# Kernel optimization log

Hardware: AMD Instinct MI355X
Metric: run time of the kernel (lower is better)

## Reference

```python
import jax, jax.numpy as jnp
import numpy as np

N_HEAD = 16


def setup_inputs() -> dict:
    key = jax.random.key(0)
    k1, k2, k3 = jax.random.split(key, 3)
    B, S, D = 2, 2048, 1024
    return {
        "hidden_states": jax.random.normal(k1, (B, S, D), dtype=jnp.float32),
        "c_attn_w": jax.random.normal(k2, (D, 3 * D), dtype=jnp.float32) * 0.02,
        "c_attn_b": jnp.zeros((3 * D,), dtype=jnp.float32),
        "c_proj_w": jax.random.normal(k3, (D, D), dtype=jnp.float32) * 0.02,
        "c_proj_b": jnp.zeros((D,), dtype=jnp.float32),
    }


def reference(hidden_states, c_attn_w, c_attn_b, c_proj_w, c_proj_b):
    B, S, D = hidden_states.shape
    H = N_HEAD
    hd = D // H
    # Fused QKV projection (Conv1D == linear with transposed weight layout)
    qkv = hidden_states @ c_attn_w + c_attn_b  # [B,S,3D]
    q, k, v = jnp.split(qkv, 3, axis=-1)
    # split heads -> [B,H,S,hd]
    q = q.reshape(B, S, H, hd).transpose(0, 2, 1, 3)
    k = k.reshape(B, S, H, hd).transpose(0, 2, 1, 3)
    v = v.reshape(B, S, H, hd).transpose(0, 2, 1, 3)
    # scaled dot-product with causal mask
    scores = jnp.einsum("bhqd,bhkd->bhqk", q, k) / jnp.asarray(hd ** 0.5, q.dtype)
    causal = jnp.tril(jnp.ones((S, S), dtype=bool))  # [S,S]
    mask_value = jnp.finfo(scores.dtype).min
    scores = jnp.where(causal[None, None, :, :], scores, mask_value)
    attn_weights = jax.nn.softmax(scores, axis=-1)  # [B,H,S,S]
    ctx = jnp.einsum("bhqk,bhkd->bhqd", attn_weights, v)  # [B,H,S,hd]
    ctx = ctx.transpose(0, 2, 1, 3).reshape(B, S, D)  # merge heads
    out = ctx @ c_proj_w + c_proj_b  # [B,S,D]
    return out
```

## Files before the change

### kernel.cpp

```cpp
#include <hip/hip_runtime.h>
#include <hip/hip_bf16.h>

typedef __attribute__((ext_vector_type(8))) short short8;
typedef __attribute__((ext_vector_type(4))) float f32x4;
typedef __attribute__((ext_vector_type(16))) float f32x16;
typedef __attribute__((ext_vector_type(4))) unsigned short u16x4;
typedef __attribute__((ext_vector_type(4))) unsigned int u32x4;

#define MFMA16(a, b, c) __builtin_amdgcn_mfma_f32_16x16x32_bf16((a), (b), (c), 0, 0, 0)
#define MFMA32(a, b, c) __builtin_amdgcn_mfma_f32_32x32x16_bf16((a), (b), (c), 0, 0, 0)

__device__ __forceinline__ unsigned short f2bf(float f) {
    union { float f; unsigned u; } v; v.f = f;
    return (unsigned short)((v.u + 0x7fffu + ((v.u >> 16) & 1u)) >> 16);
}

__device__ __forceinline__ unsigned cvtpk(float lo, float hi_) {
    unsigned r;
    asm volatile("v_cvt_pk_bf16_f32 %0, %1, %2" : "=v"(r) : "v"(lo), "v"(hi_));
    return r;
}

__global__ void cast_x_kernel(const float* __restrict__ x, ushort* __restrict__ y) {
    int i = blockIdx.x * blockDim.x + threadIdx.x;
    float4 v = ((const float4*)x)[i];
    u16x4 o = { f2bf(v.x), f2bf(v.y), f2bf(v.z), f2bf(v.w) };
    *(u16x4*)(y + (size_t)i * 4) = o;
}

__global__ void transpose_cast_kernel(const float* __restrict__ W, ushort* __restrict__ WT,
                                      int K, int N) {
    __shared__ ushort t[64][66];
    int n0 = blockIdx.x * 64, k0 = blockIdx.y * 64;
    int tn = threadIdx.x & 63, tg = threadIdx.x >> 6;
#pragma unroll
    for (int i = 0; i < 16; ++i) {
        int k = tg * 16 + i;
        t[tn][k] = f2bf(W[(size_t)(k0 + k) * N + n0 + tn]);
    }
    __syncthreads();
#pragma unroll
    for (int i = 0; i < 16; ++i) {
        int nn = tg * 16 + i;
        WT[(size_t)(n0 + nn) * K + k0 + tn] = t[nn][tn];
    }
}

#define QSCALE 0.18033688011112042f

template <int MODE>
__global__ __launch_bounds__(256, 3)
void gemm_bt_kernel(const ushort* __restrict__ A, const ushort* __restrict__ BT,
                    const float* __restrict__ bias,
                    ushort* __restrict__ Qb, ushort* __restrict__ Kb,
                    ushort* __restrict__ VT, float* __restrict__ Out,
                    int M, int N, int K) {
    __shared__ ushort Asm[2][128 * 32];
    __shared__ ushort Bsm[2][128 * 32];
    const int tid = threadIdx.x;
    const int lane = tid & 63;
    const int wv = tid >> 6;
    const int l15 = lane & 15, lg = lane >> 4;
    const int rm = (wv >> 1) * 64, cn = (wv & 1) * 64;
    const int row0 = blockIdx.y * 128, col0 = blockIdx.x * 128;

    const char* Agb = (const char*)(A + (size_t)row0 * K);
    const char* Bgb = (const char*)(BT + (size_t)col0 * K);
    const size_t rowbytes = (size_t)K * 2;

    f32x4 acc[4][4];
#pragma unroll
    for (int mi = 0; mi < 4; ++mi)
#pragma unroll
        for (int ni = 0; ni < 4; ++ni) acc[mi][ni] = f32x4{0.f, 0.f, 0.f, 0.f};

    const int sr0 = tid >> 2, sc0 = (tid & 3) ^ (sr0 & 3);
    const int sr1 = (tid + 256) >> 2, sc1 = (tid & 3) ^ (sr1 & 3);

#define GSTAGE(buf, k0_)                                                                \
    do {                                                                                \
        size_t kbyte = (size_t)(k0_)*2;                                                 \
        __builtin_amdgcn_global_load_lds(                                               \
            (const __attribute__((address_space(1))) void*)(Agb + (size_t)sr0 *         \
                rowbytes + kbyte + sc0 * 16),                                           \
            (__attribute__((address_space(3))) void*)((char*)&Asm[buf][0] + tid * 16),  \
            16, 0, 0);                                                                  \
        __builtin_amdgcn_global_load_lds(                                               \
            (const __attribute__((address_space(1))) void*)(Agb + (size_t)sr1 *         \
                rowbytes + kbyte + sc1 * 16),                                           \
            (__attribute__((address_space(3))) void*)((char*)&Asm[buf][0] + 4096 +      \
                tid * 16),                                                              \
            16, 0, 0);                                                                  \
        __builtin_amdgcn_global_load_lds(                                               \
            (const __attribute__((address_space(1))) void*)(Bgb + (size_t)sr0 *         \
                rowbytes + kbyte + sc0 * 16),                                           \
            (__attribute__((address_space(3))) void*)((char*)&Bsm[buf][0] + tid * 16),  \
            16, 0, 0);                                                                  \
        __builtin_amdgcn_global_load_lds(                                               \
            (const __attribute__((address_space(1))) void*)(Bgb + (size_t)sr1 *         \
                rowbytes + kbyte + sc1 * 16),                                           \
            (__attribute__((address_space(3))) void*)((char*)&Bsm[buf][0] + 4096 +      \
                tid * 16),                                                              \
            16, 0, 0);                                                                  \
    } while (0)

    GSTAGE(0, 0);
    __syncthreads();

    const int sw8 = (lg ^ (l15 & 3)) << 3;

    int cur = 0;
    for (int k0 = 0; k0 < K; k0 += 32) {
        if (k0 + 32 < K) GSTAGE(cur ^ 1, k0 + 32);
        short8 af[4], bf[4];
#pragma unroll
        for (int mi = 0; mi < 4; ++mi)
            af[mi] = *(const short8*)&Asm[cur][(rm + mi * 16 + l15) * 32 + sw8];
#pragma unroll
        for (int ni = 0; ni < 4; ++ni)
            bf[ni] = *(const short8*)&Bsm[cur][(cn + ni * 16 + l15) * 32 + sw8];
        __builtin_amdgcn_s_setprio(1);
#pragma unroll
        for (int mi = 0; mi < 4; ++mi)
#pragma unroll
            for (int ni = 0; ni < 4; ++ni)
                acc[mi][ni] = MFMA16(af[mi], bf[ni], acc[mi][ni]);
        __builtin_amdgcn_s_setprio(0);
        __syncthreads();
        cur ^= 1;
    }
#undef GSTAGE

    if (MODE == 0) {
        const int sect = col0 >> 10;
#pragma unroll
        for (int ni = 0; ni < 4; ++ni) {
            int col = col0 + cn + ni * 16 + l15;
            float bv = bias[col];
            int dcol = col & 1023, h = dcol >> 6, dd = dcol & 63;
#pragma unroll
            for (int mi = 0; mi < 4; ++mi) {
                int mrow0 = row0 + rm + mi * 16 + lg * 4;
                if (sect == 2) {
                    int b = mrow0 >> 11, s = mrow0 & 2047;
                    u16x4 o;
#pragma unroll
                    for (int j = 0; j < 4; ++j) o[j] = f2bf(acc[mi][ni][j] + bv);
                    *(u16x4*)&VT[((size_t)((b << 4) + h) * 64 + dd) * 2048 + s] = o;
                } else {
                    ushort* dst = sect ? Kb : Qb;
                    float sc = sect ? 1.f : QSCALE;
#pragma unroll
                    for (int j = 0; j < 4; ++j) {
                        int tok = mrow0 + j;
                        int b = tok >> 11, s = tok & 2047;
                        dst[((size_t)((b << 4) + h) * 2048 + s) * 64 + dd] =
                            f2bf((acc[mi][ni][j] + bv) * sc);
                    }
                }
            }
        }
    } else {
#pragma unroll
        for (int ni = 0; ni < 4; ++ni) {
            int col = col0 + cn + ni * 16 + l15;
            float bv = bias[col];
#pragma unroll
            for (int mi = 0; mi < 4; ++mi) {
                int mrow0 = row0 + rm + mi * 16 + lg * 4;
#pragma unroll
                for (int j = 0; j < 4; ++j)
                    Out[(size_t)(mrow0 + j) * N + col] = acc[mi][ni][j] + bv;
            }
        }
    }
}

__global__ __launch_bounds__(256)
void attn_kernel(const ushort* __restrict__ Qb, const ushort* __restrict__ Kb,
                 const ushort* __restrict__ VT, ushort* __restrict__ CTX) {
    __shared__ __align__(16) ushort Ksm[2][64 * 64];
    __shared__ __align__(16) ushort Vsm[2][64 * 64];

    const int tid = threadIdx.x;
    const int lane = tid & 63;
    const int w = tid >> 6;
    const int l31 = lane & 31;
    const int hi = lane >> 5;
    const int r7 = l31 & 7;

    const int id = blockIdx.x;
    const int xcd = id & 7, jj = id >> 3;
    const int bh = (xcd << 2) + (jj >> 4);
    const int qt = ((jj >> 5) & 1) ? (jj & 15) : 15 - (jj & 15);
    const int qw0 = qt * 128 + w * 32;
    const int qrow = qw0 + l31;

    const ushort* Qh = Qb + (size_t)bh * 2048 * 64;
    const ushort* Kh = Kb + (size_t)bh * 2048 * 64;
    const ushort* Vh = VT + (size_t)bh * 64 * 2048;

    short8 qf[4];
#pragma unroll
    for (int dc = 0; dc < 4; ++dc)
        qf[dc] = *(const short8*)&Qh[(size_t)qrow * 64 + dc * 16 + hi * 8];

    const int srow = tid >> 3;
    const int scol = tid & 7;
    const int swz8 = (scol ^ (srow & 7)) * 8;

    u32x4 kr0, kr1, vr0, vr1;

#define LDREGS(kb_)                                                                     \
    do {                                                                                \
        const ushort* kp = Kh + (size_t)((kb_) + srow) * 64 + scol * 8;                 \
        kr0 = *(const u32x4*)kp;                                                        \
        kr1 = *(const u32x4*)(kp + 32 * 64);                                            \
        const ushort* vp = Vh + (size_t)srow * 2048 + (kb_) + scol * 8;                 \
        vr0 = *(const u32x4*)vp;                                                        \
        vr1 = *(const u32x4*)(vp + (size_t)32 * 2048);                                  \
    } while (0)

#define DSWRITE(buf)                                                                    \
    do {                                                                                \
        ushort* kd = &Ksm[buf][srow * 64 + swz8];                                       \
        *(u32x4*)kd = kr0;                                                              \
        *(u32x4*)(kd + 32 * 64) = kr1;                                                  \
        ushort* vd = &Vsm[buf][srow * 64 + swz8];                                       \
        *(u32x4*)vd = vr0;                                                              \
        *(u32x4*)(vd + 32 * 64) = vr1;                                                  \
    } while (0)

    const int nc = 2 * qt + 2;
    const int cdiag = 2 * qt + (w >> 1);

    LDREGS(0);
    DSWRITE(0);
    __syncthreads();

    float mrun = -1e30f, lsum = 0.f;
    f32x16 acc0, acc1;
#pragma unroll
    for (int r = 0; r < 16; ++r) { acc0[r] = 0.f; acc1[r] = 0.f; }

    int cur = 0;
    for (int c = 0; c < nc; ++c) {
        const int kb = c * 64;
        const bool havenext = (c + 1 < nc);
        if (havenext) LDREGS(kb + 64);

        if (!(w < 2 && c == nc - 1)) {
            const ushort* Kc = &Ksm[cur][0];
            const ushort* Vc = &Vsm[cur][0];

            short8 kf0[4], kf1[4];
#pragma unroll
            for (int dc = 0; dc < 4; ++dc) {
                kf0[dc] = *(const short8*)(Kc + l31 * 64 + (((dc * 2 + hi) ^ r7) << 3));
                kf1[dc] = *(const short8*)(Kc + (32 + l31) * 64 + (((dc * 2 + hi) ^ r7) << 3));
            }

            f32x16 st0, st1;
#pragma unroll
            for (int r = 0; r < 16; ++r) { st0[r] = 0.f; st1[r] = 0.f; }
            __builtin_amdgcn_s_setprio(1);
#pragma unroll
            for (int dc = 0; dc < 4; ++dc) {
                st0 = MFMA32(kf0[dc], qf[dc], st0);
                st1 = MFMA32(kf1[dc], qf[dc], st1);
            }
            __builtin_amdgcn_s_setprio(0);

            if (c == cdiag) {
                const int base0 = kb + (hi << 2);
                const int base1 = kb + 32 + (hi << 2);
#pragma unroll
                for (int r = 0; r < 16; ++r) {
                    int k0 = base0 + ((r & 3) + 8 * (r >> 2));
                    int k1 = base1 + ((r & 3) + 8 * (r >> 2));
                    st0[r] = (k0 <= qrow) ? st0[r] : -1e30f;
                    st1[r] = (k1 <= qrow) ? st1[r] : -1e30f;
                }
            }

            short8 vg0[4], vg1[4];
#pragma unroll
            for (int g = 0; g < 4; ++g) {
                vg0[g] = *(const short8*)(Vc + l31 * 64 + (((2 * g + hi) ^ r7) << 3));
                vg1[g] = *(const short8*)(Vc + (32 + l31) * 64 + (((2 * g + hi) ^ r7) << 3));
            }

            float tm[8];
#pragma unroll
            for (int i = 0; i < 8; ++i)
                tm[i] = fmaxf(fmaxf(st0[i], st0[i + 8]), fmaxf(st1[i], st1[i + 8]));
            float tmax = fmaxf(fmaxf(fmaxf(tm[0], tm[1]), fmaxf(tm[2], tm[3])),
                               fmaxf(fmaxf(tm[4], tm[5]), fmaxf(tm[6], tm[7])));
            tmax = fmaxf(tmax, __shfl_xor(tmax, 32));

            if (!__all(tmax <= mrun + 8.0f)) {
                float mnew = fmaxf(mrun, tmax);
                float sc = exp2f(mrun - mnew);
#pragma unroll
                for (int r = 0; r < 16; ++r) { acc0[r] *= sc; acc1[r] *= sc; }
                lsum *= sc;
                mrun = mnew;
            }

#pragma unroll
            for (int r = 0; r < 16; ++r) st0[r] = exp2f(st0[r] - mrun);
#pragma unroll
            for (int r = 0; r < 16; ++r) st1[r] = exp2f(st1[r] - mrun);
            float ts[8];
#pragma unroll
            for (int i = 0; i < 8; ++i) ts[i] = st0[i] + st0[i + 8];
#pragma unroll
            for (int i = 0; i < 8; ++i) ts[i] += st1[i] + st1[i + 8];
            float tsum = ((ts[0] + ts[1]) + (ts[2] + ts[3])) +
                         ((ts[4] + ts[5]) + (ts[6] + ts[7]));
            lsum += tsum;

            if (havenext) DSWRITE(cur ^ 1);

#define MAKE_PFRAG(st, kcL, out)                                                        \
    do {                                                                                \
        unsigned c00 = cvtpk(st[8 * kcL + 0], st[8 * kcL + 1]);                         \
        unsigned c01 = cvtpk(st[8 * kcL + 2], st[8 * kcL + 3]);                         \
        unsigned c10 = cvtpk(st[8 * kcL + 4], st[8 * kcL + 5]);                         \
        unsigned c11 = cvtpk(st[8 * kcL + 6], st[8 * kcL + 7]);                         \
        unsigned e0 = hi ? c00 : c10, e1 = hi ? c01 : c11;                              \
        unsigned pa0 = e0, pb0 = e0, pa1 = e1, pb1 = e1;                                \
        asm volatile("v_permlane32_swap_b32 %0, %1" : "+v"(pa0), "+v"(pb0));            \
        asm volatile("v_permlane32_swap_b32 %0, %1" : "+v"(pa1), "+v"(pb1));            \
        unsigned rec0 = hi ? pa0 : pb0;                                                 \
        unsigned rec1 = hi ? pa1 : pb1;                                                 \
        u32x4 fw;                                                                       \
        fw.x = hi ? rec0 : c00;                                                         \
        fw.y = hi ? rec1 : c01;                                                         \
        fw.z = hi ? c10 : rec0;                                                         \
        fw.w = hi ? c11 : rec1;                                                         \
        out = __builtin_bit_cast(short8, fw);                                           \
    } while (0)

            short8 pf;
            __builtin_amdgcn_s_setprio(1);
            MAKE_PFRAG(st0, 0, pf);
            acc0 = MFMA32(vg0[0], pf, acc0);
            acc1 = MFMA32(vg1[0], pf, acc1);
            MAKE_PFRAG(st0, 1, pf);
            acc0 = MFMA32(vg0[1], pf, acc0);
            acc1 = MFMA32(vg1[1], pf, acc1);
            MAKE_PFRAG(st1, 0, pf);
            acc0 = MFMA32(vg0[2], pf, acc0);
            acc1 = MFMA32(vg1[2], pf, acc1);
            MAKE_PFRAG(st1, 1, pf);
            acc0 = MFMA32(vg0[3], pf, acc0);
            acc1 = MFMA32(vg1[3], pf, acc1);
            __builtin_amdgcn_s_setprio(0);
#undef MAKE_PFRAG
        } else {
            if (havenext) DSWRITE(cur ^ 1);
        }

        __syncthreads();
        cur ^= 1;
    }
#undef LDREGS
#undef DSWRITE

    lsum += __shfl_xor(lsum, 32);
    const float inv = 1.f / lsum;
    const int b = bh >> 4, h = bh & 15;
    const size_t tokrow = ((size_t)b * 2048 + qw0 + l31) * 1024 + (size_t)h * 64;

#define WRITE_DT(accv, dt)                                                              \
    do {                                                                                \
        _Pragma("unroll")                                                               \
        for (int q2 = 0; q2 < 4; ++q2) {                                                \
            int d0 = dt * 32 + 8 * q2 + (hi << 2);                                      \
            u16x4 o;                                                                    \
            _Pragma("unroll")                                                           \
            for (int j = 0; j < 4; ++j) o[j] = f2bf(accv[4 * q2 + j] * inv);            \
            *(u16x4*)&CTX[tokrow + d0] = o;                                             \
        }                                                                               \
    } while (0)

    WRITE_DT(acc0, 0);
    WRITE_DT(acc1, 1);
#undef WRITE_DT
}

extern "C" void kernel_launch(void* const* d_in, const int* in_sizes, int n_in,
                              void* d_out, int out_size, void* d_ws, size_t ws_size,
                              hipStream_t stream) {
    const float* X     = (const float*)d_in[0];
    const float* Wqkv  = (const float*)d_in[1];
    const float* bqkv  = (const float*)d_in[2];
    const float* Wproj = (const float*)d_in[3];
    const float* bproj = (const float*)d_in[4];
    float* Out = (float*)d_out;

    ushort* Xb     = (ushort*)d_ws;
    ushort* WqkvT  = Xb + (size_t)4096 * 1024;
    ushort* WprojT = WqkvT + (size_t)3072 * 1024;
    ushort* Qb     = WprojT + (size_t)1024 * 1024;
    ushort* Kb     = Qb + (size_t)4096 * 1024;
    ushort* VT     = Kb + (size_t)4096 * 1024;
    ushort* CTX    = VT + (size_t)4096 * 1024;

    cast_x_kernel<<<4096, 256, 0, stream>>>(X, Xb);
    transpose_cast_kernel<<<dim3(48, 16), 256, 0, stream>>>(Wqkv, WqkvT, 1024, 3072);
    transpose_cast_kernel<<<dim3(16, 16), 256, 0, stream>>>(Wproj, WprojT, 1024, 1024);
    gemm_bt_kernel<0><<<dim3(24, 32), 256, 0, stream>>>(Xb, WqkvT, bqkv, Qb, Kb, VT, nullptr,
                                                        4096, 3072, 1024);
    attn_kernel<<<512, 256, 0, stream>>>(Qb, Kb, VT, CTX);
    gemm_bt_kernel<1><<<dim3(8, 32), 256, 0, stream>>>(CTX, WprojT, bproj, nullptr, nullptr,
                                                       nullptr, Out, 4096, 1024, 1024);
}
```

Before: 130.5 us.

## Split attention KV range across two blocks and merge partial results

Each causal query tile's key range is split into two halves processed by separate blocks (1024 blocks instead of 512). Each block writes fp32 partial outputs and running max/sum to workspace, and a new merge kernel combines them into bf16 context. This is meant to balance the causal workload across more workgroups and raise occupancy, with launch bounds now requesting 4 blocks per CU. The cost is extra fp32 traffic to workspace and one more kernel launch. The P-fragment construction is also simplified to feed cvtpk outputs straight into permlane32 swaps without the select logic.

```diff
diff --git a/kernel.cpp b/kernel.cpp
--- a/kernel.cpp
+++ b/kernel.cpp
@@ -176,9 +176,11 @@
     }
 }
 
-__global__ __launch_bounds__(256)
+template <int SPLIT>
+__global__ __launch_bounds__(256, 4)
 void attn_kernel(const ushort* __restrict__ Qb, const ushort* __restrict__ Kb,
-                 const ushort* __restrict__ VT, ushort* __restrict__ CTX) {
+                 const ushort* __restrict__ VT, ushort* __restrict__ CTX,
+                 float* __restrict__ OP, float* __restrict__ ML) {
     __shared__ __align__(16) ushort Ksm[2][64 * 64];
     __shared__ __align__(16) ushort Vsm[2][64 * 64];
 
@@ -190,9 +192,23 @@
     const int r7 = l31 & 7;
 
     const int id = blockIdx.x;
-    const int xcd = id & 7, jj = id >> 3;
-    const int bh = (xcd << 2) + (jj >> 4);
-    const int qt = ((jj >> 5) & 1) ? (jj & 15) : 15 - (jj & 15);
+    int bh, qt, half, cBeg, cEnd;
+    if (SPLIT) {
+        const int xcd = id & 7, jj = id >> 3;
+        bh = (xcd << 2) + (jj & 3);
+        const int r = jj >> 2;
+        half = r >> 4;
+        const int s = r & 15;
+        qt = (s < 8) ? s : 23 - s;
+        cBeg = half * (qt + 1);
+        cEnd = cBeg + (qt + 1);
+    } else {
+        const int xcd = id & 7, jj = id >> 3;
+        bh = (xcd << 2) + (jj >> 4);
+        qt = ((jj >> 5) & 1) ? (jj & 15) : 15 - (jj & 15);
+        half = 0; cBeg = 0; cEnd = 2 * qt + 2;
+    }
+    const int nc = 2 * qt + 2;
     const int qw0 = qt * 128 + w * 32;
     const int qrow = qw0 + l31;
 
@@ -231,10 +247,9 @@
         *(u32x4*)(vd + 32 * 64) = vr1;                                                  \
     } while (0)
 
-    const int nc = 2 * qt + 2;
     const int cdiag = 2 * qt + (w >> 1);
 
-    LDREGS(0);
+    LDREGS(cBeg * 64);
     DSWRITE(0);
     __syncthreads();
 
@@ -244,9 +259,9 @@
     for (int r = 0; r < 16; ++r) { acc0[r] = 0.f; acc1[r] = 0.f; }
 
     int cur = 0;
-    for (int c = 0; c < nc; ++c) {
+    for (int c = cBeg; c < cEnd; ++c) {
         const int kb = c * 64;
-        const bool havenext = (c + 1 < nc);
+        const bool havenext = (c + 1 < cEnd);
         if (havenext) LDREGS(kb + 64);
 
         if (!(w < 2 && c == nc - 1)) {
@@ -324,21 +339,14 @@
 
 #define MAKE_PFRAG(st, kcL, out)                                                        \
     do {                                                                                \
-        unsigned c00 = cvtpk(st[8 * kcL + 0], st[8 * kcL + 1]);                         \
-        unsigned c01 = cvtpk(st[8 * kcL + 2], st[8 * kcL + 3]);                         \
-        unsigned c10 = cvtpk(st[8 * kcL + 4], st[8 * kcL + 5]);                         \
-        unsigned c11 = cvtpk(st[8 * kcL + 6], st[8 * kcL + 7]);                         \
-        unsigned e0 = hi ? c00 : c10, e1 = hi ? c01 : c11;                              \
-        unsigned pa0 = e0, pb0 = e0, pa1 = e1, pb1 = e1;                                \
-        asm volatile("v_permlane32_swap_b32 %0, %1" : "+v"(pa0), "+v"(pb0));            \
-        asm volatile("v_permlane32_swap_b32 %0, %1" : "+v"(pa1), "+v"(pb1));            \
-        unsigned rec0 = hi ? pa0 : pb0;                                                 \
-        unsigned rec1 = hi ? pa1 : pb1;                                                 \
+        unsigned a0 = cvtpk(st[8 * kcL + 0], st[8 * kcL + 1]);                          \
+        unsigned a1 = cvtpk(st[8 * kcL + 2], st[8 * kcL + 3]);                          \
+        unsigned b0 = cvtpk(st[8 * kcL + 4], st[8 * kcL + 5]);                          \
+        unsigned b1 = cvtpk(st[8 * kcL + 6], st[8 * kcL + 7]);                          \
+        asm volatile("v_permlane32_swap_b32 %0, %1" : "+v"(a0), "+v"(b0));              \
+        asm volatile("v_permlane32_swap_b32 %0, %1" : "+v"(a1), "+v"(b1));              \
         u32x4 fw;                                                                       \
-        fw.x = hi ? rec0 : c00;                                                         \
-        fw.y = hi ? rec1 : c01;                                                         \
-        fw.z = hi ? c10 : rec0;                                                         \
-        fw.w = hi ? c11 : rec1;                                                         \
+        fw.x = a0; fw.y = a1; fw.z = b0; fw.w = b1;                                     \
         out = __builtin_bit_cast(short8, fw);                                           \
     } while (0)
 
@@ -369,10 +377,31 @@
 #undef DSWRITE
 
     lsum += __shfl_xor(lsum, 32);
-    const float inv = 1.f / lsum;
-    const int b = bh >> 4, h = bh & 15;
-    const size_t tokrow = ((size_t)b * 2048 + qw0 + l31) * 1024 + (size_t)h * 64;
-
+
+    if (SPLIT) {
+        const int pidx = ((bh << 4) + qt) * 2 + half;
+        float* op = OP + (size_t)pidx * 8192 + (size_t)(w * 32 + l31) * 64;
+#define WRITE_PART(accv, dt)                                                            \
+    do {                                                                                \
+        _Pragma("unroll")                                                               \
+        for (int q2 = 0; q2 < 4; ++q2) {                                                \
+            int d0 = dt * 32 + 8 * q2 + (hi << 2);                                      \
+            f32x4 o = { accv[4 * q2 + 0], accv[4 * q2 + 1],                             \
+                        accv[4 * q2 + 2], accv[4 * q2 + 3] };                           \
+            *(f32x4*)&op[d0] = o;                                                       \
+        }                                                                               \
+    } while (0)
+        WRITE_PART(acc0, 0);
+        WRITE_PART(acc1, 1);
+#undef WRITE_PART
+        if (hi == 0) {
+            float2 r2 = { mrun, lsum };
+            *(float2*)&ML[((size_t)pidx * 128 + w * 32 + l31) * 2] = r2;
+        }
+    } else {
+        const float inv = 1.f / lsum;
+        const int b = bh >> 4, h = bh & 15;
+        const size_t tokrow = ((size_t)b * 2048 + qw0 + l31) * 1024 + (size_t)h * 64;
 #define WRITE_DT(accv, dt)                                                              \
     do {                                                                                \
         _Pragma("unroll")                                                               \
@@ -384,10 +413,38 @@
             *(u16x4*)&CTX[tokrow + d0] = o;                                             \
         }                                                                               \
     } while (0)
-
-    WRITE_DT(acc0, 0);
-    WRITE_DT(acc1, 1);
+        WRITE_DT(acc0, 0);
+        WRITE_DT(acc1, 1);
 #undef WRITE_DT
+    }
+}
+
+__global__ __launch_bounds__(256)
+void merge_kernel(const float* __restrict__ OP, const float* __restrict__ ML,
+                  ushort* __restrict__ CTX) {
+    const int bid = blockIdx.x;
+    const int bh = bid >> 4, qt = bid & 15;
+    const int tid = threadIdx.x;
+    const int row = tid >> 1, dh = (tid & 1) << 5;
+    const size_t p0 = (size_t)bid * 2, p1 = p0 + 1;
+    const float2 ml0 = *(const float2*)&ML[(p0 * 128 + row) * 2];
+    const float2 ml1 = *(const float2*)&ML[(p1 * 128 + row) * 2];
+    const float M = fmaxf(ml0.x, ml1.x);
+    const float f0 = exp2f(ml0.x - M), f1 = exp2f(ml1.x - M);
+    const float inv = 1.f / (f0 * ml0.y + f1 * ml1.y);
+    const float* a0 = OP + p0 * 8192 + (size_t)row * 64 + dh;
+    const float* a1 = OP + p1 * 8192 + (size_t)row * 64 + dh;
+    const size_t tok = (size_t)(bh >> 4) * 2048 + qt * 128 + row;
+    ushort* dst = CTX + tok * 1024 + (size_t)(bh & 15) * 64 + dh;
+#pragma unroll
+    for (int k = 0; k < 8; ++k) {
+        f32x4 v0 = *(const f32x4*)(a0 + 4 * k);
+        f32x4 v1 = *(const f32x4*)(a1 + 4 * k);
+        u16x4 o;
+#pragma unroll
+        for (int j = 0; j < 4; ++j) o[j] = f2bf((f0 * v0[j] + f1 * v1[j]) * inv);
+        *(u16x4*)(dst + 4 * k) = o;
+    }
 }
 
 extern "C" void kernel_launch(void* const* d_in, const int* in_sizes, int n_in,
@@ -407,13 +464,21 @@
     ushort* Kb     = Qb + (size_t)4096 * 1024;
     ushort* VT     = Kb + (size_t)4096 * 1024;
     ushort* CTX    = VT + (size_t)4096 * 1024;
+    float* OP = (float*)((char*)d_ws + (size_t)48 * 1024 * 1024);
+    float* ML = OP + (size_t)1024 * 128 * 64;
+    const size_t NEED = (size_t)(48 + 32 + 1) * 1024 * 1024;
 
     cast_x_kernel<<<4096, 256, 0, stream>>>(X, Xb);
     transpose_cast_kernel<<<dim3(48, 16), 256, 0, stream>>>(Wqkv, WqkvT, 1024, 3072);
     transpose_cast_kernel<<<dim3(16, 16), 256, 0, stream>>>(Wproj, WprojT, 1024, 1024);
     gemm_bt_kernel<0><<<dim3(24, 32), 256, 0, stream>>>(Xb, WqkvT, bqkv, Qb, Kb, VT, nullptr,
                                                         4096, 3072, 1024);
-    attn_kernel<<<512, 256, 0, stream>>>(Qb, Kb, VT, CTX);
+    if (ws_size >= NEED) {
+        attn_kernel<1><<<1024, 256, 0, stream>>>(Qb, Kb, VT, CTX, OP, ML);
+        merge_kernel<<<512, 256, 0, stream>>>(OP, ML, CTX);
+    } else {
+        attn_kernel<0><<<512, 256, 0, stream>>>(Qb, Kb, VT, CTX, nullptr, nullptr);
+    }
     gemm_bt_kernel<1><<<dim3(8, 32), 256, 0, stream>>>(CTX, WprojT, bproj, nullptr, nullptr,
                                                        nullptr, Out, 4096, 1024, 1024);
 }
```

After: 163.9 us. 25.6% more time.
